# Kernel optimization log

Hardware: AMD Instinct MI355X
Metric: run time of the kernel (lower is better)

Reference implementation:

```python
import jax, jax.numpy as jnp
import numpy as np

NEG_SLOPE = 0.2  # PyG GATv2Conv default


def with_self_loops(edge_index, n):
    loop = jnp.arange(n, dtype=edge_index.dtype)
    src = jnp.concatenate([edge_index[0], loop])
    dst = jnp.concatenate([edge_index[1], loop])
    return src, dst


def gatv2(x, src, dst, Wl, bl, Wr, br, att, bias):
    """PyG GATv2Conv (eval mode, concat=True, add_self_loops done by caller).
    x: [N, F_in]; att: [H, C]. Returns [N, H*C]."""
    N = x.shape[0]
    H, C = att.shape
    xl = (x @ Wl + bl).reshape(N, H, C)  # lin_l(x): source-side transform
    xr = (x @ Wr + br).reshape(N, H, C)  # lin_r(x): target-side transform
    s = jax.nn.leaky_relu(xl[src] + xr[dst], NEG_SLOPE)      # [E,H,C]
    logit = jnp.einsum('ehc,hc->eh', s, att)                 # [E,H]
    m = jax.ops.segment_max(logit, dst, num_segments=N)      # stable softmax per target
    e = jnp.exp(logit - m[dst])
    den = jax.ops.segment_sum(e, dst, num_segments=N)
    alpha = e / (den[dst] + 1e-16)                           # [E,H]
    out = jax.ops.segment_sum(alpha[:, :, None] * xl[src], dst, num_segments=N)
    return out.reshape(N, H * C) + bias


def setup_inputs() -> dict:
    N, E = 20000, 320000        # agent nodes / edges
    M, EM = 40000, 400000       # lane nodes / edges
    B, L = 64, 50               # focal agents, centerline length
    SEQ, INC, HID, HEADS, OUT = 50, 2, 32, 4, 60
    H4 = HID * HEADS
    key = jax.random.key(0)
    ks = list(jax.random.split(key, 48))
    kit = iter(ks)

    def p(shape):
        return jax.random.normal(next(kit), shape, jnp.float32) * 0.05

    inp = {
        'x': jax.random.normal(next(kit), (N, SEQ, INC), jnp.float32),
        'edge_index': jax.random.randint(next(kit), (2, E), 0, N),
        'lane_x': jax.random.normal(next(kit), (M, 2), jnp.float32),
        'lane_edge_index': jax.random.randint(next(kit), (2, EM), 0, M),
        'batch': jnp.sort(jax.random.randint(next(kit), (N,), 0, B)),
        'focal_idx': jax.random.randint(next(kit), (B,), 0, N),
        'centerlines': jax.random.normal(next(kit), (B, L, 2), jnp.float32),
        # agent embedding
        'ae_W': p((SEQ * INC, HID)), 'ae_b': p((HID,)),
        # agent subgraph conv1 / conv2
        'a1_Wl': p((HID, H4)), 'a1_bl': p((H4,)), 'a1_Wr': p((HID, H4)), 'a1_br': p((H4,)), 'a1_att': p((HEADS, HID)), 'a1_b': p((H4,)),
        'a2_Wl': p((H4, H4)), 'a2_bl': p((H4,)), 'a2_Wr': p((H4, H4)), 'a2_br': p((H4,)), 'a2_att': p((HEADS, HID)), 'a2_b': p((H4,)),
        # map embedding + map subgraph
        'me_W': p((2, HID)), 'me_b': p((HID,)),
        'm1_Wl': p((HID, H4)), 'm1_bl': p((H4,)), 'm1_Wr': p((HID, H4)), 'm1_br': p((H4,)), 'm1_att': p((HEADS, HID)), 'm1_b': p((H4,)),
        'm2_Wl': p((H4, H4)), 'm2_bl': p((H4,)), 'm2_Wr': p((H4, H4)), 'm2_br': p((H4,)), 'm2_att': p((HEADS, HID)), 'm2_b': p((H4,)),
        # centerline processor
        'cl_W': p((2, HID)), 'cl_b': p((HID,)),
        # global graph (heads=1)
        'g_Wl': p((H4, HID)), 'g_bl': p((HID,)), 'g_Wr': p((H4, HID)), 'g_br': p((HID,)), 'g_att': p((1, HID)), 'g_b': p((HID,)),
        # output head
        'fc_W': p((2 * HID, OUT)), 'fc_b': p((OUT,)),
    }
    return inp


def reference(x, edge_index, lane_x, lane_edge_index, batch, focal_idx, centerlines,
              ae_W, ae_b,
              a1_Wl, a1_bl, a1_Wr, a1_br, a1_att, a1_b,
              a2_Wl, a2_bl, a2_Wr, a2_br, a2_att, a2_b,
              me_W, me_b,
              m1_Wl, m1_bl, m1_Wr, m1_br, m1_att, m1_b,
              m2_Wl, m2_bl, m2_Wr, m2_br, m2_att, m2_b,
              cl_W, cl_b,
              g_Wl, g_bl, g_Wr, g_br, g_att, g_b,
              fc_W, fc_b):
    N = x.shape[0]
    M = lane_x.shape[0]
    # agent branch
    agent_x = jax.nn.relu(x.reshape(N, -1) @ ae_W + ae_b)
    a_src, a_dst = with_self_loops(edge_index, N)
    h = jax.nn.relu(gatv2(agent_x, a_src, a_dst, a1_Wl, a1_bl, a1_Wr, a1_br, a1_att, a1_b))
    agent_features = jax.nn.relu(gatv2(h, a_src, a_dst, a2_Wl, a2_bl, a2_Wr, a2_br, a2_att, a2_b))  # [N,128]
    # map branch (output unused downstream in original, computed for faithfulness)
    map_x = jax.nn.relu(lane_x @ me_W + me_b)
    m_src, m_dst = with_self_loops(lane_edge_index, M)
    hm = jax.nn.relu(gatv2(map_x, m_src, m_dst, m1_Wl, m1_bl, m1_Wr, m1_br, m1_att, m1_b))
    map_features = jax.nn.relu(gatv2(hm, m_src, m_dst, m2_Wl, m2_bl, m2_Wr, m2_br, m2_att, m2_b))
    _ = map_features  # global_mean_pool results are dead code in the original forward
    # global graph over agent features (heads=1)
    global_features = jax.nn.relu(gatv2(agent_features, a_src, a_dst, g_Wl, g_bl, g_Wr, g_br, g_att, g_b))  # [N,32]
    focal = global_features[focal_idx]  # [B,32]
    # centerlines: per-polyline mean then linear (no relu, as in original)
    cl_feat = jnp.mean(centerlines, axis=1) @ cl_W + cl_b  # [B,32]
    combined = jnp.concatenate([focal, cl_feat], axis=1)
    return combined @ fc_W + fc_b
```

## Files before the change

### kernel.cpp

```cpp
#include <hip/hip_runtime.h>
#include <hip/hip_bf16.h>
#include <hip/hip_fp16.h>
#include <math.h>

typedef __hip_bfloat16 bf16;
#define NEG_SLOPE 0.2f

typedef _Float16 f16x8 __attribute__((ext_vector_type(8)));
typedef float f32x4 __attribute__((ext_vector_type(4)));

#define NSEG 25
struct Seg { const void* src; int n; int off; };
struct Tab { Seg s[NSEG]; };

__device__ __forceinline__ float ldconv(const void* src, int i, int f32mode) {
    return f32mode ? ((const float*)src)[i]
                   : __bfloat162float(((const bf16*)src)[i]);
}

__global__ void k_convert(Tab tab, float* __restrict__ dst,
                          const unsigned short* __restrict__ xdet, int* __restrict__ flag,
                          const int* __restrict__ srcArr, const int* __restrict__ dstArr,
                          int E, int N,
                          int* __restrict__ deg, int* __restrict__ csrF,
                          int* __restrict__ spillD, int* __restrict__ spillS,
                          int* __restrict__ spillCnt,
                          const void* a2WlS, const void* a2WrS,
                          const void* gWlS, const void* gWrS,
                          __half* __restrict__ a2Wlt, __half* __restrict__ a2Wrt,
                          __half* __restrict__ gWlt, __half* __restrict__ gWrt) {
    __shared__ int cnt;
    if (threadIdx.x == 0) cnt = 0;
    __syncthreads();
    int local = 0;
    for (int i = threadIdx.x; i < 2048; i += blockDim.x) {
        unsigned short w = xdet[2 * i];
        int e = (w >> 7) & 0xFF;
        if (e >= 0x90) local++;
    }
    atomicAdd(&cnt, local);
    __syncthreads();
    int f32mode = (cnt > 100) ? 1 : 0;
    if (blockIdx.x == 0 && threadIdx.x == 0) flag[0] = f32mode;

    int gid = blockIdx.x * blockDim.x + threadIdx.x;
    int gsz = gridDim.x * blockDim.x;
    for (int s = 0; s < NSEG; s++) {
        Seg sg = tab.s[s];
        for (int i = gid; i < sg.n; i += gsz) {
            dst[sg.off + i] = ldconv(sg.src, i, f32mode);
        }
    }
    for (int i = gid; i < 128 * 128; i += gsz) {
        int k = i >> 7, j = i & 127;
        a2Wlt[(size_t)j * 128 + k] = __float2half(ldconv(a2WlS, i, f32mode));
        a2Wrt[(size_t)j * 128 + k] = __float2half(ldconv(a2WrS, i, f32mode));
    }
    for (int i = gid; i < 128 * 32; i += gsz) {
        int k = i >> 5, j = i & 31;
        gWlt[(size_t)j * 128 + k] = __float2half(ldconv(gWlS, i, f32mode));
        gWrt[(size_t)j * 128 + k] = __float2half(ldconv(gWrS, i, f32mode));
    }
    int EA = E + N;
    for (int e = gid; e < EA; e += gsz) {
        int d, s;
        if (e < E) { d = dstArr[e]; s = srcArr[e]; } else { d = s = e - E; }
        int r = atomicAdd(&deg[d], 1);
        if (r < 64) {
            csrF[(size_t)d * 64 + r] = s;
        } else {
            int o = atomicAdd(spillCnt, 1);
            spillD[o] = d; spillS[o] = s;
        }
    }
}

__launch_bounds__(256)
__global__ void k_embedlin(const void* __restrict__ xraw, const int* __restrict__ flag,
                           int N,
                           const float* __restrict__ aeW, const float* __restrict__ aeb,
                           const float* __restrict__ Wl, const float* __restrict__ bl,
                           const float* __restrict__ Wr, const float* __restrict__ br,
                           __half* __restrict__ outl, float* __restrict__ outr) {
    __shared__ float xs[100 * 36];
    __shared__ float axs[32 * 36];
    constexpr int NTP = 36;
    int t = threadIdx.x, nb = blockIdx.x * 32;
    if (flag[0]) {
        const float4* x4 = (const float4*)xraw;
        for (int idx = t; idx < 32 * 25; idx += 256) {
            int node = idx / 25, k4 = idx % 25;
            float4 v = x4[(size_t)(nb + node) * 25 + k4];
            xs[(k4 * 4 + 0) * NTP + node] = v.x;
            xs[(k4 * 4 + 1) * NTP + node] = v.y;
            xs[(k4 * 4 + 2) * NTP + node] = v.z;
            xs[(k4 * 4 + 3) * NTP + node] = v.w;
        }
    } else {
        const ushort4* xu = (const ushort4*)xraw;
        for (int idx = t; idx < 32 * 25; idx += 256) {
            int node = idx / 25, k4 = idx % 25;
            ushort4 u = xu[(size_t)(nb + node) * 25 + k4];
            xs[(k4 * 4 + 0) * NTP + node] = __uint_as_float((unsigned)u.x << 16);
            xs[(k4 * 4 + 1) * NTP + node] = __uint_as_float((unsigned)u.y << 16);
            xs[(k4 * 4 + 2) * NTP + node] = __uint_as_float((unsigned)u.z << 16);
            xs[(k4 * 4 + 3) * NTP + node] = __uint_as_float((unsigned)u.w << 16);
        }
    }
    __syncthreads();
    {
        int j = t & 31, g0 = t >> 5;
        float a0 = 0.f, a1 = 0.f, a2 = 0.f, a3 = 0.f;
        #pragma unroll 10
        for (int k = 0; k < 100; k++) {
            float w = aeW[k * 32 + j];
            const float4 xv = *(const float4*)&xs[k * NTP + g0 * 4];
            a0 += w * xv.x; a1 += w * xv.y; a2 += w * xv.z; a3 += w * xv.w;
        }
        float bj = aeb[j];
        axs[j * NTP + g0 * 4 + 0] = fmaxf(a0 + bj, 0.f);
        axs[j * NTP + g0 * 4 + 1] = fmaxf(a1 + bj, 0.f);
        axs[j * NTP + g0 * 4 + 2] = fmaxf(a2 + bj, 0.f);
        axs[j * NTP + g0 * 4 + 3] = fmaxf(a3 + bj, 0.f);
    }
    __syncthreads();
    {
        int j = t & 63, g0 = t >> 6;
        float aL0[2][4], aL1[2][4], aR0[2][4], aR1[2][4];
        #pragma unroll
        for (int g = 0; g < 2; g++)
            #pragma unroll
            for (int c = 0; c < 4; c++) { aL0[g][c]=0.f; aL1[g][c]=0.f; aR0[g][c]=0.f; aR1[g][c]=0.f; }
        #pragma unroll 4
        for (int k = 0; k < 32; k++) {
            float wl0 = Wl[k * 128 + j];
            float wl1 = Wl[k * 128 + j + 64];
            float wr0 = Wr[k * 128 + j];
            float wr1 = Wr[k * 128 + j + 64];
            #pragma unroll
            for (int g = 0; g < 2; g++) {
                const float4 xv = *(const float4*)&axs[k * NTP + (g0 + g * 4) * 4];
                aL0[g][0] += wl0 * xv.x; aL0[g][1] += wl0 * xv.y; aL0[g][2] += wl0 * xv.z; aL0[g][3] += wl0 * xv.w;
                aL1[g][0] += wl1 * xv.x; aL1[g][1] += wl1 * xv.y; aL1[g][2] += wl1 * xv.z; aL1[g][3] += wl1 * xv.w;
                aR0[g][0] += wr0 * xv.x; aR0[g][1] += wr0 * xv.y; aR0[g][2] += wr0 * xv.z; aR0[g][3] += wr0 * xv.w;
                aR1[g][0] += wr1 * xv.x; aR1[g][1] += wr1 * xv.y; aR1[g][2] += wr1 * xv.z; aR1[g][3] += wr1 * xv.w;
            }
        }
        float bl0 = bl[j], bl1 = bl[j + 64], br0 = br[j], br1 = br[j + 64];
        #pragma unroll
        for (int g = 0; g < 2; g++) {
            int n0 = nb + (g0 + g * 4) * 4;
            #pragma unroll
            for (int c = 0; c < 4; c++) {
                size_t row = (size_t)(n0 + c) * 128;
                outl[row + j]      = __float2half(aL0[g][c] + bl0);
                outl[row + j + 64] = __float2half(aL1[g][c] + bl1);
                outr[row + j]      = aR0[g][c] + br0;
                outr[row + j + 64] = aR1[g][c] + br1;
            }
        }
    }
}

__device__ __forceinline__ void gat_proc(float4 raw, bool valid,
                                         const float* xrd, const float* av,
                                         float* acc, float& sm) {
    const __half2* h = (const __half2*)&raw;
    float v[8];
    float2 f;
    f = __half22float2(h[0]); v[0] = f.x; v[1] = f.y;
    f = __half22float2(h[1]); v[2] = f.x; v[3] = f.y;
    f = __half22float2(h[2]); v[4] = f.x; v[5] = f.y;
    f = __half22float2(h[3]); v[6] = f.x; v[7] = f.y;
    float p = 0.f;
    #pragma unroll
    for (int c = 0; c < 8; c++) {
        float u = v[c] + xrd[c];
        u = (u > 0.f) ? u : NEG_SLOPE * u;
        p += u * av[c];
    }
    p += __shfl_xor(p, 1);
    p += __shfl_xor(p, 2);
    p += __shfl_xor(p, 4);
    p += __shfl_xor(p, 8);
    float w = __expf(fminf(p, 80.f));
    if (!valid) w = 0.f;
    sm += w;
    #pragma unroll
    for (int c = 0; c < 8; c++) acc[c] += w * v[c];
}

__device__ __forceinline__ void gat16_to_lds(__half* xsh,
                                             const __half* __restrict__ xl,
                                             const float* __restrict__ xr,
                                             const float* __restrict__ att,
                                             const int* __restrict__ deg,
                                             const int* __restrict__ csrF,
                                             const int* __restrict__ spillD,
                                             const int* __restrict__ spillS,
                                             const int* __restrict__ spillCnt,
                                             const float* __restrict__ bias,
                                             int d, int node) {
    int t = threadIdx.x;
    int lane = t & 63;
    int sub = lane & 15;
    int lb = lane & 48;
    float av[8];
    {
        const float4* t4 = (const float4*)(att + sub * 8);
        float4 c = t4[0], e = t4[1];
        av[0]=c.x; av[1]=c.y; av[2]=c.z; av[3]=c.w;
        av[4]=e.x; av[5]=e.y; av[6]=e.z; av[7]=e.w;
    }
    bool ok = d >= 0;
    int cnt = ok ? deg[d] : 0;
    int cmain = cnt < 64 ? cnt : 64;
    size_t i0 = (size_t)(ok ? d : 0) * 64;

    float xrd[8];
    #pragma unroll
    for (int c = 0; c < 8; c++) xrd[c] = 0.f;
    if (ok) {
        const float4* p4 = (const float4*)(xr + (size_t)d * 128 + sub * 8);
        float4 a = p4[0], b = p4[1];
        xrd[0]=a.x; xrd[1]=a.y; xrd[2]=a.z; xrd[3]=a.w;
        xrd[4]=b.x; xrd[5]=b.y; xrd[6]=b.z; xrd[7]=b.w;
    }
    float acc[8];
    #pragma unroll
    for (int c = 0; c < 8; c++) acc[c] = 0.f;
    float sm = 0.f;

    int myv = (sub < cmain) ? csrF[i0 + sub] : 0;
    for (int c0 = 0; c0 < cmain; c0 += 16) {
        int myv_nxt = (c0 + 16 + sub < cmain) ? csrF[i0 + c0 + 16 + sub] : 0;
        int rem = min(cmain - c0, 16);
        for (int k = 0; k < rem; k += 4) {
            int s0 = __shfl(myv, lb + k + 0);
            int s1 = __shfl(myv, lb + k + 1);
            int s2 = __shfl(myv, lb + k + 2);
            int s3 = __shfl(myv, lb + k + 3);
            float4 r0 = *(const float4*)(xl + (size_t)s0 * 128 + sub * 8);
            float4 r1 = *(const float4*)(xl + (size_t)s1 * 128 + sub * 8);
            float4 r2 = *(const float4*)(xl + (size_t)s2 * 128 + sub * 8);
            float4 r3 = *(const float4*)(xl + (size_t)s3 * 128 + sub * 8);
            gat_proc(r0, true,        xrd, av, acc, sm);
            gat_proc(r1, k + 1 < rem, xrd, av, acc, sm);
            gat_proc(r2, k + 2 < rem, xrd, av, acc, sm);
            gat_proc(r3, k + 3 < rem, xrd, av, acc, sm);
        }
        myv = myv_nxt;
    }
    if (cnt > 64) {
        int stot = *spillCnt;
        for (int j = 0; j < stot; j++) {
            if (spillD[j] == d) {
                float4 r = *(const float4*)(xl + (size_t)spillS[j] * 128 + sub * 8);
                gat_proc(r, true, xrd, av, acc, sm);
            }
        }
    }

    int ch = sub * 8;
    if (ok) {
        float inv = 1.f / (sm + 1e-16f);
        #pragma unroll
        for (int c = 0; c < 8; c += 2) {
            __half2 hv;
            hv.x = __float2half(fmaxf(acc[c]     * inv + bias[ch + c],     0.f));
            hv.y = __float2half(fmaxf(acc[c + 1] * inv + bias[ch + c + 1], 0.f));
            *(__half2*)&xsh[node * 136 + ch + c] = hv;
        }
    } else {
        #pragma unroll
        for (int c = 0; c < 8; c += 2)
            *(__half2*)&xsh[node * 136 + ch + c] = __half2{__half(0.f), __half(0.f)};
    }
}

__launch_bounds__(256)
__global__ void k_gatlin(const __half* __restrict__ xl, const float* __restrict__ xr,
                         const float* __restrict__ att,
                         const int* __restrict__ deg, const int* __restrict__ csrF,
                         const int* __restrict__ spillD, const int* __restrict__ spillS,
                         const int* __restrict__ spillCnt,
                         const float* __restrict__ bias,
                         const __half* __restrict__ Wlt, const float* __restrict__ bl,
                         const __half* __restrict__ Wrt, const float* __restrict__ br,
                         __half* __restrict__ outl, float* __restrict__ outr, int N,
                         const int* __restrict__ focal, int B,
                         int* __restrict__ L, int* __restrict__ Lcnt, int GT) {
    if (blockIdx.x >= GT) {
        int t = threadIdx.x;
        if (t < B) {
            int f = focal[t];
            int cf = deg[f];
            int cm = cf < 64 ? cf : 64;
            int base = atomicAdd(Lcnt, cf);
            for (int j = 0; j < cm; j++) L[base + j] = csrF[(size_t)f * 64 + j];
            if (cf > 64) {
                int k = cm;
                int stot = *spillCnt;
                for (int j = 0; j < stot; j++)
                    if (spillD[j] == f) L[base + k++] = spillS[j];
            }
        }
        return;
    }
    __shared__ __align__(16) __half xsh[16 * 136];
    int nb = blockIdx.x * 16;
    int t = threadIdx.x;
    int lane = t & 63, wv = t >> 6;
    int quad = lane >> 4, n16 = lane & 15;
    {
        int node = wv * 4 + quad;
        int dd = nb + node;
        gat16_to_lds(xsh, xl, xr, att, deg, csrF, spillD, spillS, spillCnt,
                     bias, (dd < N) ? dd : -1, node);
    }
    __syncthreads();

    f16x8 a[4];
    #pragma unroll
    for (int kt = 0; kt < 4; kt++)
        a[kt] = *(const f16x8*)&xsh[n16 * 136 + kt * 32 + quad * 8];

    int j0 = wv * 32;
    f32x4 aL0 = {0.f,0.f,0.f,0.f}, aL1 = {0.f,0.f,0.f,0.f};
    f32x4 aR0 = {0.f,0.f,0.f,0.f}, aR1 = {0.f,0.f,0.f,0.f};
    #pragma unroll
    for (int kt = 0; kt < 4; kt++) {
        int ko = kt * 32 + quad * 8;
        f16x8 b0 = *(const f16x8*)&Wlt[(size_t)(j0 + n16) * 128 + ko];
        f16x8 b1 = *(const f16x8*)&Wlt[(size_t)(j0 + 16 + n16) * 128 + ko];
        f16x8 b2 = *(const f16x8*)&Wrt[(size_t)(j0 + n16) * 128 + ko];
        f16x8 b3 = *(const f16x8*)&Wrt[(size_t)(j0 + 16 + n16) * 128 + ko];
        aL0 = __builtin_amdgcn_mfma_f32_16x16x32_f16(a[kt], b0, aL0, 0, 0, 0);
        aL1 = __builtin_amdgcn_mfma_f32_16x16x32_f16(a[kt], b1, aL1, 0, 0, 0);
        aR0 = __builtin_amdgcn_mfma_f32_16x16x32_f16(a[kt], b2, aR0, 0, 0, 0);
        aR1 = __builtin_amdgcn_mfma_f32_16x16x32_f16(a[kt], b3, aR1, 0, 0, 0);
    }
    float blj0 = bl[j0 + n16], blj1 = bl[j0 + 16 + n16];
    float brj0 = br[j0 + n16], brj1 = br[j0 + 16 + n16];
    #pragma unroll
    for (int r = 0; r < 4; r++) {
        int node = quad * 4 + r;
        if (nb + node >= N) continue;
        size_t row = (size_t)(nb + node) * 128;
        outl[row + j0 + n16]      = __float2half(aL0[r] + blj0);
        outl[row + j0 + 16 + n16] = __float2half(aL1[r] + blj1);
        outr[row + j0 + n16]      = aR0[r] + brj0;
        outr[row + j0 + 16 + n16] = aR1[r] + brj1;
    }
}

__launch_bounds__(256)
__global__ void k_gatling(const __half* __restrict__ xl, const float* __restrict__ xr,
                          const float* __restrict__ att,
                          const int* __restrict__ deg, const int* __restrict__ csrF,
                          const int* __restrict__ spillD, const int* __restrict__ spillS,
                          const int* __restrict__ spillCnt,
                          const float* __restrict__ bias,
                          const __half* __restrict__ Wlt, const float* __restrict__ bl,
                          const __half* __restrict__ Wrt, const float* __restrict__ br,
                          __half* __restrict__ outl, float* __restrict__ outr,
                          const int* __restrict__ L, const int* __restrict__ Lcnt) {
    __shared__ __align__(16) __half xsh[16 * 136];
    int total = *Lcnt;
    int t = threadIdx.x;
    int lane = t & 63, wv = t >> 6;
    int quad = lane >> 4, n16 = lane & 15;

    for (int tile = blockIdx.x; tile * 16 < total; tile += gridDim.x) {
        if (tile != (int)blockIdx.x) __syncthreads();
        int node = wv * 4 + quad;
        int idx = tile * 16 + node;
        int d = (idx < total) ? L[idx] : -1;
        gat16_to_lds(xsh, xl, xr, att, deg, csrF, spillD, spillS, spillCnt,
                     bias, d, node);
        __syncthreads();

        f16x8 a[4];
        #pragma unroll
        for (int kt = 0; kt < 4; kt++)
            a[kt] = *(const f16x8*)&xsh[n16 * 136 + kt * 32 + quad * 8];

        const __half* Wt = (wv < 2) ? Wlt : Wrt;
        int j0 = (wv & 1) * 16;
        f32x4 accv = {0.f,0.f,0.f,0.f};
        #pragma unroll
        for (int kt = 0; kt < 4; kt++) {
            f16x8 b = *(const f16x8*)&Wt[(size_t)(j0 + n16) * 128 + kt * 32 + quad * 8];
            accv = __builtin_amdgcn_mfma_f32_16x16x32_f16(a[kt], b, accv, 0, 0, 0);
        }
        float bj = ((wv < 2) ? bl : br)[j0 + n16];
        #pragma unroll
        for (int r = 0; r < 4; r++) {
            int nn = quad * 4 + r;
            int gidx = tile * 16 + nn;
            if (gidx >= total) continue;
            int gd = L[gidx];
            size_t row = (size_t)gd * 32;
            if (wv < 2) outl[row + j0 + n16] = __float2half(accv[r] + bj);
            else        outr[row + j0 + n16] = accv[r] + bj;
        }
    }
}

__launch_bounds__(64)
__global__ void k_tailf(const __half* __restrict__ xl, const float* __restrict__ xr,
                        const float* __restrict__ att,
                        const int* __restrict__ deg, const int* __restrict__ csrF,
                        const int* __restrict__ spillD, const int* __restrict__ spillS,
                        const int* __restrict__ spillCnt,
                        const float* __restrict__ gb, const int* __restrict__ focal,
                        const float* __restrict__ clf, const float* __restrict__ clW,
                        const float* __restrict__ clb, const float* __restrict__ fcW,
                        const float* __restrict__ fcb, void* __restrict__ out,
                        const int* __restrict__ flag) {
    __shared__ float comb[64];
    __shared__ float ssb[2];
    int b = blockIdx.x;
    int t = threadIdx.x;
    int d = focal[b];
    int grp = t >> 3, sub = t & 7;
    int cnt = deg[d];
    int cm = cnt < 64 ? cnt : 64;
    size_t i0 = (size_t)d * 64;

    float xrd[4], av[4], acc[4];
    {
        float4 a = *(const float4*)(xr + (size_t)d * 32 + sub * 4);
        xrd[0]=a.x; xrd[1]=a.y; xrd[2]=a.z; xrd[3]=a.w;
        float4 c = *(const float4*)(att + sub * 4);
        av[0]=c.x; av[1]=c.y; av[2]=c.z; av[3]=c.w;
    }
    #pragma unroll
    for (int c = 0; c < 4; c++) acc[c] = 0.f;
    float sm = 0.f;

    auto edge = [&](int s) {
        float2 raw = *(const float2*)(xl + (size_t)s * 32 + sub * 4);
        const __half2* h = (const __half2*)&raw;
        float v[4];
        float2 f;
        f = __half22float2(h[0]); v[0] = f.x; v[1] = f.y;
        f = __half22float2(h[1]); v[2] = f.x; v[3] = f.y;
        float p = 0.f;
        #pragma unroll
        for (int c = 0; c < 4; c++) {
            float u = v[c] + xrd[c];
            u = (u > 0.f) ? u : NEG_SLOPE * u;
            p += u * av[c];
        }
        p += __shfl_xor(p, 1);
        p += __shfl_xor(p, 2);
        p += __shfl_xor(p, 4);
        float w = __expf(fminf(p, 80.f));
        sm += w;
        #pragma unroll
        for (int c = 0; c < 4; c++) acc[c] += w * v[c];
    };
    for (int i = grp; i < cm; i += 8) edge(csrF[i0 + i]);
    if (cnt > 64) {
        int stot = *spillCnt;
        for (int i = grp; i < stot; i += 8)
            if (spillD[i] == d) edge(spillS[i]);
    }
    sm += __shfl_xor(sm, 8); sm += __shfl_xor(sm, 16); sm += __shfl_xor(sm, 32);
    #pragma unroll
    for (int c = 0; c < 4; c++) {
        acc[c] += __shfl_xor(acc[c], 8);
        acc[c] += __shfl_xor(acc[c], 16);
        acc[c] += __shfl_xor(acc[c], 32);
    }
    if (grp == 0) {
        float inv = 1.f / (sm + 1e-16f);
        #pragma unroll
        for (int c = 0; c < 4; c++)
            comb[sub * 4 + c] = fmaxf(acc[c] * inv + gb[sub * 4 + c], 0.f);
    }
    if (t < 2) {
        float s = 0.f;
        for (int l = 0; l < 50; l++) s += clf[(size_t)b * 100 + l * 2 + t];
        ssb[t] = s / 50.f;
    }
    __syncthreads();
    if (t < 32) comb[32 + t] = ssb[0] * clW[t] + ssb[1] * clW[32 + t] + clb[t];
    __syncthreads();
    if (t < 60) {
        float a2 = fcb[t];
        #pragma unroll 16
        for (int k = 0; k < 64; k++) a2 += comb[k] * fcW[k * 60 + t];
        if (flag[0]) ((float*)out)[b * 60 + t] = a2;
        else ((bf16*)out)[b * 60 + t] = __float2bfloat16(a2);
    }
}

extern "C" void kernel_launch(void* const* d_in, const int* in_sizes, int n_in,
                              void* d_out, int out_size, void* d_ws, size_t ws_size,
                              hipStream_t stream) {
    const int* edge  = (const int*)d_in[1];
    const int* focal = (const int*)d_in[5];

    const int N = in_sizes[0] / 100;
    const int E = in_sizes[1] / 2;
    const int B = in_sizes[5];
    const int EA = E + N;
    const int* srcArr = edge;
    const int* dstArr = edge + E;

    const int idxs[NSEG] = {7,8,9,10,11,12,13,14,15,16,17,18,19,20,
                            35,36,37,38,39,40,41,42,43,44, 6};
    float* base = (float*)d_ws;
    int* flag = (int*)base;
    float* wf = base + 16;
    Tab tab;
    int off[NSEG];
    int o = 0;
    for (int i = 0; i < NSEG; i++) {
        tab.s[i].src = d_in[idxs[i]];
        tab.s[i].n   = in_sizes[idxs[i]];
        tab.s[i].off = o;
        off[i] = o;
        o += in_sizes[idxs[i]];
    }
    const float* aeW  = wf + off[0],  *aeb  = wf + off[1];
    const float* a1Wl = wf + off[2],  *a1bl = wf + off[3];
    const float* a1Wr = wf + off[4],  *a1br = wf + off[5];
    const float* a1att= wf + off[6],  *a1b  = wf + off[7];
    const float* a2bl = wf + off[9];
    const float* a2br = wf + off[11];
    const float* a2att= wf + off[12], *a2b  = wf + off[13];
    const float* clW  = wf + off[14], *clb  = wf + off[15];
    const float* gbl  = wf + off[17];
    const float* gbr  = wf + off[19];
    const float* gatt = wf + off[20], *gb   = wf + off[21];
    const float* fcW  = wf + off[22], *fcb  = wf + off[23];
    const float* clf  = wf + off[24];

    float* p = wf + o + ((4 - (o & 3)) & 3);
    size_t N128 = (size_t)N * 128;
    __half* hxl1 = (__half*)p;      p += (size_t)N * 64;
    float* fB1  = p;                p += N128;
    __half* hxl2 = (__half*)p;      p += (size_t)N * 64;
    float* fB2  = p;                p += N128;
    int* deg    = (int*)p;
    int* st     = deg + N;
    int* csrF   = st + 32;
    int* spillD = csrF + (size_t)N * 64;
    int* spillS = spillD + EA;
    uintptr_t up = (uintptr_t)(spillS + EA);
    up = (up + 15) & ~(uintptr_t)15;
    __half* a2Wlt = (__half*)up;
    __half* a2Wrt = a2Wlt + 16384;
    __half* gWlt  = a2Wrt + 16384;
    __half* gWrt  = gWlt + 4096;
    int* Lbuf = (int*)(gWrt + 4096);
    int* Lcnt = st + 30;
    int* spillCnt = st + 29;

    const int EB = N / 32;
    const int GT = (N + 15) / 16;

    hipMemsetAsync(deg, 0, (size_t)(N + 32) * sizeof(int), stream);
    k_convert<<<256, 256, 0, stream>>>(tab, wf, (const unsigned short*)d_in[0], flag,
                                       srcArr, dstArr, E, N, deg, csrF,
                                       spillD, spillS, spillCnt,
                                       d_in[15], d_in[17], d_in[37], d_in[39],
                                       a2Wlt, a2Wrt, gWlt, gWrt);
    k_embedlin<<<EB, 256, 0, stream>>>(d_in[0], flag, N, aeW, aeb,
                                       a1Wl, a1bl, a1Wr, a1br, hxl1, fB1);
    k_gatlin<<<GT + 1, 256, 0, stream>>>(hxl1, fB1, a1att, deg, csrF,
                                         spillD, spillS, spillCnt, a1b,
                                         a2Wlt, a2bl, a2Wrt, a2br, hxl2, fB2, N,
                                         focal, B, Lbuf, Lcnt, GT);
    k_gatling<<<128, 256, 0, stream>>>(hxl2, fB2, a2att, deg, csrF,
                                       spillD, spillS, spillCnt, a2b,
                                       gWlt, gbl, gWrt, gbr, hxl1, fB1, Lbuf, Lcnt);
    k_tailf<<<B, 64, 0, stream>>>(hxl1, fB1, gatt, deg, csrF,
                                  spillD, spillS, spillCnt, gb, focal,
                                  clf, clW, clb, fcW, fcb, d_out, flag);
}
```

Baseline: 234.0 us.

## Fuse convert with embedding and fuse last GAT layer into focal tail kernel

Merges the weight-conversion/CSR-build kernel with the agent embedding+linear kernel into one launch, with embed blocks reading raw weights through ldconv directly. Folds the global-graph linear transform and the tail attention into one per-focal-agent kernel that computes neighbor projections into LDS on the fly, removing the focal-neighbor list build and two launches. This trades launch and intermediate-buffer overhead for redundant neighbor work across focal blocks. It also leaves only 64 blocks for the last stage and serializes the neighbor tiles inside each block.

Measured after the change: 234.2 us (median of 2 runs). No clear change (+0.1%).

```diff
diff --git a/kernel.cpp b/kernel.cpp
--- a/kernel.cpp
+++ b/kernel.cpp
@@ -18,75 +18,77 @@
                    : __bfloat162float(((const bf16*)src)[i]);
 }
 
-__global__ void k_convert(Tab tab, float* __restrict__ dst,
-                          const unsigned short* __restrict__ xdet, int* __restrict__ flag,
-                          const int* __restrict__ srcArr, const int* __restrict__ dstArr,
-                          int E, int N,
-                          int* __restrict__ deg, int* __restrict__ csrF,
-                          int* __restrict__ spillD, int* __restrict__ spillS,
-                          int* __restrict__ spillCnt,
-                          const void* a2WlS, const void* a2WrS,
-                          const void* gWlS, const void* gWrS,
-                          __half* __restrict__ a2Wlt, __half* __restrict__ a2Wrt,
-                          __half* __restrict__ gWlt, __half* __restrict__ gWrt) {
+__launch_bounds__(256)
+__global__ void k_convembed(Tab tab, float* __restrict__ dst,
+                            const unsigned short* __restrict__ xdet, int* __restrict__ flag,
+                            const int* __restrict__ srcArr, const int* __restrict__ dstArr,
+                            int E, int N,
+                            int* __restrict__ deg, int* __restrict__ csrF,
+                            int* __restrict__ spillD, int* __restrict__ spillS,
+                            int* __restrict__ spillCnt,
+                            const void* a2WlS, const void* a2WrS,
+                            const void* gWlS, const void* gWrS,
+                            __half* __restrict__ a2Wlt, __half* __restrict__ a2Wrt,
+                            __half* __restrict__ gWlt, __half* __restrict__ gWrt,
+                            const void* __restrict__ xraw,
+                            const void* aeWr, const void* aebr,
+                            const void* Wlr, const void* blr,
+                            const void* Wrr, const void* brr,
+                            __half* __restrict__ outl, float* __restrict__ outr,
+                            int CB) {
     __shared__ int cnt;
     if (threadIdx.x == 0) cnt = 0;
     __syncthreads();
-    int local = 0;
-    for (int i = threadIdx.x; i < 2048; i += blockDim.x) {
-        unsigned short w = xdet[2 * i];
-        int e = (w >> 7) & 0xFF;
-        if (e >= 0x90) local++;
-    }
-    atomicAdd(&cnt, local);
-    __syncthreads();
-    int f32mode = (cnt > 100) ? 1 : 0;
-    if (blockIdx.x == 0 && threadIdx.x == 0) flag[0] = f32mode;
-
-    int gid = blockIdx.x * blockDim.x + threadIdx.x;
-    int gsz = gridDim.x * blockDim.x;
-    for (int s = 0; s < NSEG; s++) {
-        Seg sg = tab.s[s];
-        for (int i = gid; i < sg.n; i += gsz) {
-            dst[sg.off + i] = ldconv(sg.src, i, f32mode);
-        }
-    }
-    for (int i = gid; i < 128 * 128; i += gsz) {
-        int k = i >> 7, j = i & 127;
-        a2Wlt[(size_t)j * 128 + k] = __float2half(ldconv(a2WlS, i, f32mode));
-        a2Wrt[(size_t)j * 128 + k] = __float2half(ldconv(a2WrS, i, f32mode));
-    }
-    for (int i = gid; i < 128 * 32; i += gsz) {
-        int k = i >> 5, j = i & 31;
-        gWlt[(size_t)j * 128 + k] = __float2half(ldconv(gWlS, i, f32mode));
-        gWrt[(size_t)j * 128 + k] = __float2half(ldconv(gWrS, i, f32mode));
-    }
-    int EA = E + N;
-    for (int e = gid; e < EA; e += gsz) {
-        int d, s;
-        if (e < E) { d = dstArr[e]; s = srcArr[e]; } else { d = s = e - E; }
-        int r = atomicAdd(&deg[d], 1);
-        if (r < 64) {
-            csrF[(size_t)d * 64 + r] = s;
-        } else {
-            int o = atomicAdd(spillCnt, 1);
-            spillD[o] = d; spillS[o] = s;
-        }
-    }
-}
-
-__launch_bounds__(256)
-__global__ void k_embedlin(const void* __restrict__ xraw, const int* __restrict__ flag,
-                           int N,
-                           const float* __restrict__ aeW, const float* __restrict__ aeb,
-                           const float* __restrict__ Wl, const float* __restrict__ bl,
-                           const float* __restrict__ Wr, const float* __restrict__ br,
-                           __half* __restrict__ outl, float* __restrict__ outr) {
+    {
+        int local = 0;
+        for (int i = threadIdx.x; i < 2048; i += blockDim.x) {
+            unsigned short w = xdet[2 * i];
+            int e = (w >> 7) & 0xFF;
+            if (e >= 0x90) local++;
+        }
+        atomicAdd(&cnt, local);
+    }
+    __syncthreads();
+    int f32m = (cnt > 100) ? 1 : 0;
+    if (blockIdx.x == 0 && threadIdx.x == 0) flag[0] = f32m;
+
+    if (blockIdx.x < CB) {
+        int gid = blockIdx.x * blockDim.x + threadIdx.x;
+        int gsz = CB * blockDim.x;
+        for (int s = 0; s < NSEG; s++) {
+            Seg sg = tab.s[s];
+            for (int i = gid; i < sg.n; i += gsz)
+                dst[sg.off + i] = ldconv(sg.src, i, f32m);
+        }
+        for (int i = gid; i < 128 * 128; i += gsz) {
+            int k = i >> 7, j = i & 127;
+            a2Wlt[(size_t)j * 128 + k] = __float2half(ldconv(a2WlS, i, f32m));
+            a2Wrt[(size_t)j * 128 + k] = __float2half(ldconv(a2WrS, i, f32m));
+        }
+        for (int i = gid; i < 128 * 32; i += gsz) {
+            int k = i >> 5, j = i & 31;
+            gWlt[(size_t)j * 128 + k] = __float2half(ldconv(gWlS, i, f32m));
+            gWrt[(size_t)j * 128 + k] = __float2half(ldconv(gWrS, i, f32m));
+        }
+        int EA = E + N;
+        for (int e = gid; e < EA; e += gsz) {
+            int d, s;
+            if (e < E) { d = dstArr[e]; s = srcArr[e]; } else { d = s = e - E; }
+            int r = atomicAdd(&deg[d], 1);
+            if (r < 64) {
+                csrF[(size_t)d * 64 + r] = s;
+            } else {
+                int o = atomicAdd(spillCnt, 1);
+                spillD[o] = d; spillS[o] = s;
+            }
+        }
+        return;
+    }
     __shared__ float xs[100 * 36];
     __shared__ float axs[32 * 36];
     constexpr int NTP = 36;
-    int t = threadIdx.x, nb = blockIdx.x * 32;
-    if (flag[0]) {
+    int t = threadIdx.x, nb = (blockIdx.x - CB) * 32;
+    if (f32m) {
         const float4* x4 = (const float4*)xraw;
         for (int idx = t; idx < 32 * 25; idx += 256) {
             int node = idx / 25, k4 = idx % 25;
@@ -113,11 +115,11 @@
         float a0 = 0.f, a1 = 0.f, a2 = 0.f, a3 = 0.f;
         #pragma unroll 10
         for (int k = 0; k < 100; k++) {
-            float w = aeW[k * 32 + j];
+            float w = ldconv(aeWr, k * 32 + j, f32m);
             const float4 xv = *(const float4*)&xs[k * NTP + g0 * 4];
             a0 += w * xv.x; a1 += w * xv.y; a2 += w * xv.z; a3 += w * xv.w;
         }
-        float bj = aeb[j];
+        float bj = ldconv(aebr, j, f32m);
         axs[j * NTP + g0 * 4 + 0] = fmaxf(a0 + bj, 0.f);
         axs[j * NTP + g0 * 4 + 1] = fmaxf(a1 + bj, 0.f);
         axs[j * NTP + g0 * 4 + 2] = fmaxf(a2 + bj, 0.f);
@@ -133,10 +135,10 @@
             for (int c = 0; c < 4; c++) { aL0[g][c]=0.f; aL1[g][c]=0.f; aR0[g][c]=0.f; aR1[g][c]=0.f; }
         #pragma unroll 4
         for (int k = 0; k < 32; k++) {
-            float wl0 = Wl[k * 128 + j];
-            float wl1 = Wl[k * 128 + j + 64];
-            float wr0 = Wr[k * 128 + j];
-            float wr1 = Wr[k * 128 + j + 64];
+            float wl0 = ldconv(Wlr, k * 128 + j, f32m);
+            float wl1 = ldconv(Wlr, k * 128 + j + 64, f32m);
+            float wr0 = ldconv(Wrr, k * 128 + j, f32m);
+            float wr1 = ldconv(Wrr, k * 128 + j + 64, f32m);
             #pragma unroll
             for (int g = 0; g < 2; g++) {
                 const float4 xv = *(const float4*)&axs[k * NTP + (g0 + g * 4) * 4];
@@ -146,7 +148,8 @@
                 aR1[g][0] += wr1 * xv.x; aR1[g][1] += wr1 * xv.y; aR1[g][2] += wr1 * xv.z; aR1[g][3] += wr1 * xv.w;
             }
         }
-        float bl0 = bl[j], bl1 = bl[j + 64], br0 = br[j], br1 = br[j + 64];
+        float bl0 = ldconv(blr, j, f32m), bl1 = ldconv(blr, j + 64, f32m);
+        float br0 = ldconv(brr, j, f32m), br1 = ldconv(brr, j + 64, f32m);
         #pragma unroll
         for (int g = 0; g < 2; g++) {
             int n0 = nb + (g0 + g * 4) * 4;
@@ -287,26 +290,7 @@
                          const float* __restrict__ bias,
                          const __half* __restrict__ Wlt, const float* __restrict__ bl,
                          const __half* __restrict__ Wrt, const float* __restrict__ br,
-                         __half* __restrict__ outl, float* __restrict__ outr, int N,
-                         const int* __restrict__ focal, int B,
-                         int* __restrict__ L, int* __restrict__ Lcnt, int GT) {
-    if (blockIdx.x >= GT) {
-        int t = threadIdx.x;
-        if (t < B) {
-            int f = focal[t];
-            int cf = deg[f];
-            int cm = cf < 64 ? cf : 64;
-            int base = atomicAdd(Lcnt, cf);
-            for (int j = 0; j < cm; j++) L[base + j] = csrF[(size_t)f * 64 + j];
-            if (cf > 64) {
-                int k = cm;
-                int stot = *spillCnt;
-                for (int j = 0; j < stot; j++)
-                    if (spillD[j] == f) L[base + k++] = spillS[j];
-            }
-        }
-        return;
-    }
+                         __half* __restrict__ outl, float* __restrict__ outr, int N) {
     __shared__ __align__(16) __half xsh[16 * 136];
     int nb = blockIdx.x * 16;
     int t = threadIdx.x;
@@ -355,7 +339,7 @@
 }
 
 __launch_bounds__(256)
-__global__ void k_gatling(const __half* __restrict__ xl, const float* __restrict__ xr,
+__global__ void k_gatfuse(const __half* __restrict__ xl, const float* __restrict__ xr,
                           const float* __restrict__ att,
                           const int* __restrict__ deg, const int* __restrict__ csrF,
                           const int* __restrict__ spillD, const int* __restrict__ spillS,
@@ -363,127 +347,150 @@
                           const float* __restrict__ bias,
                           const __half* __restrict__ Wlt, const float* __restrict__ bl,
                           const __half* __restrict__ Wrt, const float* __restrict__ br,
-                          __half* __restrict__ outl, float* __restrict__ outr,
-                          const int* __restrict__ L, const int* __restrict__ Lcnt) {
+                          const float* __restrict__ gatt, const float* __restrict__ gb,
+                          const int* __restrict__ focal,
+                          const float* __restrict__ clf, const float* __restrict__ clW,
+                          const float* __restrict__ clb, const float* __restrict__ fcW,
+                          const float* __restrict__ fcb, void* __restrict__ out,
+                          const int* __restrict__ flag) {
     __shared__ __align__(16) __half xsh[16 * 136];
-    int total = *Lcnt;
+    __shared__ __align__(16) __half glx[64][32];
+    __shared__ float xrf[32];
+    __shared__ int slotbuf[64];
+    __shared__ int spillCur;
+    __shared__ float comb[64];
+    __shared__ float ssb[2];
+
+    int b = blockIdx.x;
+    int f = focal[b];
+    int cf = deg[f];
+    int cm = cf < 64 ? cf : 64;
     int t = threadIdx.x;
     int lane = t & 63, wv = t >> 6;
     int quad = lane >> 4, n16 = lane & 15;
-
-    for (int tile = blockIdx.x; tile * 16 < total; tile += gridDim.x) {
-        if (tile != (int)blockIdx.x) __syncthreads();
+    if (t == 0) spillCur = 0;
+
+    {
         int node = wv * 4 + quad;
-        int idx = tile * 16 + node;
-        int d = (idx < total) ? L[idx] : -1;
         gat16_to_lds(xsh, xl, xr, att, deg, csrF, spillD, spillS, spillCnt,
-                     bias, d, node);
+                     bias, (node == 0) ? f : -1, node);
         __syncthreads();
-
         f16x8 a[4];
         #pragma unroll
         for (int kt = 0; kt < 4; kt++)
             a[kt] = *(const f16x8*)&xsh[n16 * 136 + kt * 32 + quad * 8];
-
-        const __half* Wt = (wv < 2) ? Wlt : Wrt;
-        int j0 = (wv & 1) * 16;
-        f32x4 accv = {0.f,0.f,0.f,0.f};
-        #pragma unroll
-        for (int kt = 0; kt < 4; kt++) {
-            f16x8 b = *(const f16x8*)&Wt[(size_t)(j0 + n16) * 128 + kt * 32 + quad * 8];
-            accv = __builtin_amdgcn_mfma_f32_16x16x32_f16(a[kt], b, accv, 0, 0, 0);
-        }
-        float bj = ((wv < 2) ? bl : br)[j0 + n16];
-        #pragma unroll
-        for (int r = 0; r < 4; r++) {
-            int nn = quad * 4 + r;
-            int gidx = tile * 16 + nn;
-            if (gidx >= total) continue;
-            int gd = L[gidx];
-            size_t row = (size_t)gd * 32;
-            if (wv < 2) outl[row + j0 + n16] = __float2half(accv[r] + bj);
-            else        outr[row + j0 + n16] = accv[r] + bj;
-        }
-    }
-}
-
-__launch_bounds__(64)
-__global__ void k_tailf(const __half* __restrict__ xl, const float* __restrict__ xr,
-                        const float* __restrict__ att,
-                        const int* __restrict__ deg, const int* __restrict__ csrF,
-                        const int* __restrict__ spillD, const int* __restrict__ spillS,
-                        const int* __restrict__ spillCnt,
-                        const float* __restrict__ gb, const int* __restrict__ focal,
-                        const float* __restrict__ clf, const float* __restrict__ clW,
-                        const float* __restrict__ clb, const float* __restrict__ fcW,
-                        const float* __restrict__ fcb, void* __restrict__ out,
-                        const int* __restrict__ flag) {
-    __shared__ float comb[64];
-    __shared__ float ssb[2];
-    int b = blockIdx.x;
-    int t = threadIdx.x;
-    int d = focal[b];
-    int grp = t >> 3, sub = t & 7;
-    int cnt = deg[d];
-    int cm = cnt < 64 ? cnt : 64;
-    size_t i0 = (size_t)d * 64;
-
-    float xrd[4], av[4], acc[4];
-    {
-        float4 a = *(const float4*)(xr + (size_t)d * 32 + sub * 4);
-        xrd[0]=a.x; xrd[1]=a.y; xrd[2]=a.z; xrd[3]=a.w;
-        float4 c = *(const float4*)(att + sub * 4);
-        av[0]=c.x; av[1]=c.y; av[2]=c.z; av[3]=c.w;
-    }
-    #pragma unroll
-    for (int c = 0; c < 4; c++) acc[c] = 0.f;
+        if (wv >= 2) {
+            int j0 = (wv & 1) * 16;
+            f32x4 accv = {0.f,0.f,0.f,0.f};
+            #pragma unroll
+            for (int kt = 0; kt < 4; kt++) {
+                f16x8 bb = *(const f16x8*)&Wrt[(size_t)(j0 + n16) * 128 + kt * 32 + quad * 8];
+                accv = __builtin_amdgcn_mfma_f32_16x16x32_f16(a[kt], bb, accv, 0, 0, 0);
+            }
+            if (quad == 0) xrf[j0 + n16] = accv[0] + br[j0 + n16];
+        }
+        __syncthreads();
+    }
+
+    int grp = t >> 3, sub8 = t & 7;
+    float xrd4[4], av4[4], acc4[4];
     float sm = 0.f;
-
-    auto edge = [&](int s) {
-        float2 raw = *(const float2*)(xl + (size_t)s * 32 + sub * 4);
-        const __half2* h = (const __half2*)&raw;
-        float v[4];
-        float2 f;
-        f = __half22float2(h[0]); v[0] = f.x; v[1] = f.y;
-        f = __half22float2(h[1]); v[2] = f.x; v[3] = f.y;
-        float p = 0.f;
+    if (t < 64) {
+        float4 a = *(const float4*)&xrf[sub8 * 4];
+        xrd4[0]=a.x; xrd4[1]=a.y; xrd4[2]=a.z; xrd4[3]=a.w;
+        float4 c = *(const float4*)(gatt + sub8 * 4);
+        av4[0]=c.x; av4[1]=c.y; av4[2]=c.z; av4[3]=c.w;
+        #pragma unroll
+        for (int c2 = 0; c2 < 4; c2++) acc4[c2] = 0.f;
+    }
+
+    for (int c0 = 0; c0 < cf; c0 += 64) {
+        int cn = cf - c0; if (cn > 64) cn = 64;
+        __syncthreads();
+        if (t < cn && c0 + t < cm) slotbuf[t] = csrF[(size_t)f * 64 + c0 + t];
+        __syncthreads();
+        if (t == 0 && c0 + cn > cm) {
+            int k = cm - c0; if (k < 0) k = 0;
+            int stot = *spillCnt;
+            while (k < cn) {
+                while (spillCur < stot && spillD[spillCur] != f) spillCur++;
+                if (spillCur < stot) slotbuf[k++] = spillS[spillCur++];
+                else slotbuf[k++] = f;
+            }
+        }
+        __syncthreads();
+        for (int tb = 0; tb < cn; tb += 16) {
+            int node = wv * 4 + quad;
+            int si = tb + node;
+            int d = (si < cn) ? slotbuf[si] : -1;
+            gat16_to_lds(xsh, xl, xr, att, deg, csrF, spillD, spillS, spillCnt,
+                         bias, d, node);
+            __syncthreads();
+            f16x8 a[4];
+            #pragma unroll
+            for (int kt = 0; kt < 4; kt++)
+                a[kt] = *(const f16x8*)&xsh[n16 * 136 + kt * 32 + quad * 8];
+            if (wv < 2) {
+                int j0 = (wv & 1) * 16;
+                f32x4 accv = {0.f,0.f,0.f,0.f};
+                #pragma unroll
+                for (int kt = 0; kt < 4; kt++) {
+                    f16x8 bb = *(const f16x8*)&Wlt[(size_t)(j0 + n16) * 128 + kt * 32 + quad * 8];
+                    accv = __builtin_amdgcn_mfma_f32_16x16x32_f16(a[kt], bb, accv, 0, 0, 0);
+                }
+                float bj = bl[j0 + n16];
+                #pragma unroll
+                for (int r = 0; r < 4; r++)
+                    glx[tb + quad * 4 + r][j0 + n16] = __float2half(accv[r] + bj);
+            }
+            __syncthreads();
+        }
+        if (t < 64) {
+            for (int j = c0 + grp; j < c0 + cn; j += 8) {
+                float2 raw = *(const float2*)&glx[j - c0][sub8 * 4];
+                const __half2* h = (const __half2*)&raw;
+                float v[4];
+                float2 fx;
+                fx = __half22float2(h[0]); v[0] = fx.x; v[1] = fx.y;
+                fx = __half22float2(h[1]); v[2] = fx.x; v[3] = fx.y;
+                float p = 0.f;
+                #pragma unroll
+                for (int c = 0; c < 4; c++) {
+                    float u = v[c] + xrd4[c];
+                    u = (u > 0.f) ? u : NEG_SLOPE * u;
+                    p += u * av4[c];
+                }
+                p += __shfl_xor(p, 1);
+                p += __shfl_xor(p, 2);
+                p += __shfl_xor(p, 4);
+                float w = __expf(fminf(p, 80.f));
+                sm += w;
+                #pragma unroll
+                for (int c = 0; c < 4; c++) acc4[c] += w * v[c];
+            }
+        }
+    }
+    __syncthreads();
+
+    if (t < 64) {
+        sm += __shfl_xor(sm, 8); sm += __shfl_xor(sm, 16); sm += __shfl_xor(sm, 32);
         #pragma unroll
         for (int c = 0; c < 4; c++) {
-            float u = v[c] + xrd[c];
-            u = (u > 0.f) ? u : NEG_SLOPE * u;
-            p += u * av[c];
-        }
-        p += __shfl_xor(p, 1);
-        p += __shfl_xor(p, 2);
-        p += __shfl_xor(p, 4);
-        float w = __expf(fminf(p, 80.f));
-        sm += w;
-        #pragma unroll
-        for (int c = 0; c < 4; c++) acc[c] += w * v[c];
-    };
-    for (int i = grp; i < cm; i += 8) edge(csrF[i0 + i]);
-    if (cnt > 64) {
-        int stot = *spillCnt;
-        for (int i = grp; i < stot; i += 8)
-            if (spillD[i] == d) edge(spillS[i]);
-    }
-    sm += __shfl_xor(sm, 8); sm += __shfl_xor(sm, 16); sm += __shfl_xor(sm, 32);
-    #pragma unroll
-    for (int c = 0; c < 4; c++) {
-        acc[c] += __shfl_xor(acc[c], 8);
-        acc[c] += __shfl_xor(acc[c], 16);
-        acc[c] += __shfl_xor(acc[c], 32);
-    }
-    if (grp == 0) {
-        float inv = 1.f / (sm + 1e-16f);
-        #pragma unroll
-        for (int c = 0; c < 4; c++)
-            comb[sub * 4 + c] = fmaxf(acc[c] * inv + gb[sub * 4 + c], 0.f);
-    }
-    if (t < 2) {
-        float s = 0.f;
-        for (int l = 0; l < 50; l++) s += clf[(size_t)b * 100 + l * 2 + t];
-        ssb[t] = s / 50.f;
+            acc4[c] += __shfl_xor(acc4[c], 8);
+            acc4[c] += __shfl_xor(acc4[c], 16);
+            acc4[c] += __shfl_xor(acc4[c], 32);
+        }
+        if (grp == 0) {
+            float inv = 1.f / (sm + 1e-16f);
+            #pragma unroll
+            for (int c = 0; c < 4; c++)
+                comb[sub8 * 4 + c] = fmaxf(acc4[c] * inv + gb[sub8 * 4 + c], 0.f);
+        }
+        if (t < 2) {
+            float s = 0.f;
+            for (int l = 0; l < 50; l++) s += clf[(size_t)b * 100 + l * 2 + t];
+            ssb[t] = s / 50.f;
+        }
     }
     __syncthreads();
     if (t < 32) comb[32 + t] = ssb[0] * clW[t] + ssb[1] * clW[32 + t] + clb[t];
@@ -525,9 +532,6 @@
         off[i] = o;
         o += in_sizes[idxs[i]];
     }
-    const float* aeW  = wf + off[0],  *aeb  = wf + off[1];
-    const float* a1Wl = wf + off[2],  *a1bl = wf + off[3];
-    const float* a1Wr = wf + off[4],  *a1br = wf + off[5];
     const float* a1att= wf + off[6],  *a1b  = wf + off[7];
     const float* a2bl = wf + off[9];
     const float* a2br = wf + off[11];
@@ -556,29 +560,26 @@
     __half* a2Wrt = a2Wlt + 16384;
     __half* gWlt  = a2Wrt + 16384;
     __half* gWrt  = gWlt + 4096;
-    int* Lbuf = (int*)(gWrt + 4096);
-    int* Lcnt = st + 30;
     int* spillCnt = st + 29;
 
+    const int CB = 256;
     const int EB = N / 32;
     const int GT = (N + 15) / 16;
 
     hipMemsetAsync(deg, 0, (size_t)(N + 32) * sizeof(int), stream);
-    k_convert<<<256, 256, 0, stream>>>(tab, wf, (const unsigned short*)d_in[0], flag,
-                                       srcArr, dstArr, E, N, deg, csrF,
-                                       spillD, spillS, spillCnt,
-                                       d_in[15], d_in[17], d_in[37], d_in[39],
-                                       a2Wlt, a2Wrt, gWlt, gWrt);
-    k_embedlin<<<EB, 256, 0, stream>>>(d_in[0], flag, N, aeW, aeb,
-                                       a1Wl, a1bl, a1Wr, a1br, hxl1, fB1);
-    k_gatlin<<<GT + 1, 256, 0, stream>>>(hxl1, fB1, a1att, deg, csrF,
-                                         spillD, spillS, spillCnt, a1b,
-                                         a2Wlt, a2bl, a2Wrt, a2br, hxl2, fB2, N,
-                                         focal, B, Lbuf, Lcnt, GT);
-    k_gatling<<<128, 256, 0, stream>>>(hxl2, fB2, a2att, deg, csrF,
-                                       spillD, spillS, spillCnt, a2b,
-                                       gWlt, gbl, gWrt, gbr, hxl1, fB1, Lbuf, Lcnt);
-    k_tailf<<<B, 64, 0, stream>>>(hxl1, fB1, gatt, deg, csrF,
-                                  spillD, spillS, spillCnt, gb, focal,
-                                  clf, clW, clb, fcW, fcb, d_out, flag);
-}
+    k_convembed<<<CB + EB, 256, 0, stream>>>(tab, wf, (const unsigned short*)d_in[0],
+                                             flag, srcArr, dstArr, E, N,
+                                             deg, csrF, spillD, spillS, spillCnt,
+                                             d_in[15], d_in[17], d_in[37], d_in[39],
+                                             a2Wlt, a2Wrt, gWlt, gWrt,
+                                             d_in[0], d_in[7], d_in[8],
+                                             d_in[9], d_in[10], d_in[11], d_in[12],
+                                             hxl1, fB1, CB);
+    k_gatlin<<<GT, 256, 0, stream>>>(hxl1, fB1, a1att, deg, csrF,
+                                     spillD, spillS, spillCnt, a1b,
+                                     a2Wlt, a2bl, a2Wrt, a2br, hxl2, fB2, N);
+    k_gatfuse<<<B, 256, 0, stream>>>(hxl2, fB2, a2att, deg, csrF,
+                                     spillD, spillS, spillCnt, a2b,
+                                     gWlt, gbl, gWrt, gbr, gatt, gb, focal,
+                                     clf, clW, clb, fcW, fcb, d_out, flag);
+}
```
